# Kernel optimization log

Hardware: AMD Instinct MI355X
Metric: run time of the kernel (lower is better)

Reference implementation:

```python
import jax, jax.numpy as jnp
import numpy as np

LEAK = 0.01  # PyTorch LeakyReLU default negative_slope


def _leaky(x):
    return jnp.where(x >= 0, x, LEAK * x)


def _sim1(x, ws):
    # 7-layer 1x1-conv MLP applied per pixel; x: (..., Cin, H, W)
    n = len(ws)
    for i, w in enumerate(ws):
        x = jnp.einsum('oc,...chw->...ohw', w, x)
        if i < n - 1:
            x = _leaky(x)
    return x


def setup_inputs() -> dict:
    key = jax.random.key(0)
    ks = jax.random.split(key, 9)
    B, C, S, K = 8, 256, 15, 17
    d = {
        'template_feature': jax.random.normal(ks[0], (B, C, S, S), jnp.float32),
        'candidate_feature': jax.random.normal(ks[1], (B, C, S + K - 1, S + K - 1), jnp.float32),
    }
    chans = [(C, 2 * C), (C // 2, C), (C // 4, C // 2), (C // 8, C // 4),
             (C // 16, C // 8), (C // 32, C // 16), (1, C // 32)]
    for i, (o, c) in enumerate(chans):
        # kaiming_normal_ fan_out for a 1x1 conv: std = sqrt(2/out_channels)
        d[f'w{i}'] = jax.random.normal(ks[2 + i], (o, c), jnp.float32) * np.sqrt(2.0 / o).astype(np.float32)
    return d


def reference(template_feature, candidate_feature, w0, w1, w2, w3, w4, w5, w6):
    ws = (w0, w1, w2, w3, w4, w5, w6)
    B, C, S, _ = template_feature.shape
    K = 17  # sliding-window grid (31-15+1)

    # ---- template branch ----
    t_mean = jnp.mean(template_feature, axis=(-2, -1), keepdims=True)
    rep = jnp.concatenate([jnp.broadcast_to(t_mean, template_feature.shape),
                           template_feature], axis=1)  # (B, 2C, S, S)
    w = _sim1(rep, ws)  # (B, 1, S, S)
    wn = jax.nn.softmax(w.reshape(B, 1, -1), axis=2).reshape(B, 1, S, S)
    common_template = jnp.sum(template_feature * wn, axis=(-2, -1)).reshape(B, C, 1, 1)

    # ---- candidate branch: im2col of 15x15 windows over 31x31 -> 17x17 grid ----
    ii = jnp.arange(S)[:, None] + jnp.arange(K)[None, :]  # (S, K): in-window + window-offset
    # cand_all[b,c,i,j,p,q] = candidate[b,c, i+p, j+q]  -> (B, C, S, S, K, K)
    cand_all = candidate_feature[:, :, ii[:, None, :, None], ii[None, :, None, :]]
    c_mean = jnp.mean(cand_all, axis=(2, 3), keepdims=True)  # divide by S*S as in original
    rep_c = jnp.concatenate([jnp.broadcast_to(c_mean, cand_all.shape), cand_all], axis=1)  # (B, 2C, S, S, K, K)
    rep_c = jnp.transpose(rep_c, (0, 4, 5, 1, 2, 3))  # (B, K, K, 2C, S, S)
    w_c = _sim1(rep_c, ws)  # (B, K, K, 1, S, S)
    wcn = jax.nn.softmax(w_c.reshape(B, K, K, 1, -1), axis=-1).reshape(B, K, K, 1, S, S)
    wcn = jnp.transpose(wcn, (0, 3, 4, 5, 1, 2))  # (B, 1, S, S, K, K)
    common_candidate = jnp.sum(cand_all * wcn, axis=(2, 3))  # (B, C, K, K)

    return common_template, common_candidate
```

## Files before the change

kernel.cpp:

```cpp
#include <hip/hip_runtime.h>

typedef _Float16 half_t;
typedef half_t h2    __attribute__((ext_vector_type(2)));
typedef half_t half4 __attribute__((ext_vector_type(4)));
typedef half_t half8 __attribute__((ext_vector_type(8)));
typedef __fp16 pk16x2 __attribute__((ext_vector_type(2)));
typedef float  f32x4 __attribute__((ext_vector_type(4)));
typedef float  f32x2 __attribute__((ext_vector_type(2)));

static __device__ __forceinline__ half4 pack4(f32x4 a) {
  pk16x2 lo = __builtin_amdgcn_cvt_pkrtz(a[0], a[1]);
  pk16x2 hi = __builtin_amdgcn_cvt_pkrtz(a[2], a[3]);
  half4 h;
  h[0] = lo[0]; h[1] = lo[1]; h[2] = hi[0]; h[3] = hi[1];
  return h;
}

constexpr int B_  = 8;
constexpr int S_  = 15;
constexpr int K_  = 17;
constexpr int P_  = 31;
constexpr int SS_ = 225;
constexpr int PP_ = 961;
constexpr int KK_ = 289;

constexpr int NROW_C = B_ * PP_;
constexpr int NROW_T = B_ * SS_;
constexpr int NROW   = NROW_C + NROW_T;

constexpr int NW0H = 512 * 256;
constexpr int NF16 = 128*256 + 64*128 + 32*64;

constexpr size_t OFF_GOUT = 0;
constexpr size_t OFF_ROWS = OFF_GOUT + (size_t)NROW * 256;
constexpr size_t OFF_M0   = OFF_ROWS + (size_t)B_ * 31 * 17 * 256;
constexpr size_t OFF_TM0  = OFF_M0   + (size_t)B_ * KK_ * 256;
constexpr size_t OFF_F16  = OFF_TM0  + (size_t)B_ * 256;

constexpr int X0B  = 0;
constexpr int X1B  = 32768;
constexpr int X3TB = 32768;
constexpr int Y4B  = 41984;
constexpr int SMB  = 49152;
constexpr int REDB = 50112;
constexpr int W4B  = 50176;
constexpr int W5B  = 52480;
constexpr int W6B  = 53120;
constexpr int ROWB = 53152;
constexpr int LDSB = 53632;

__global__ __launch_bounds__(256) void featT_kernel(
    const float* __restrict__ templ, const float* __restrict__ cand,
    half_t* __restrict__ inarrh)
{
  __shared__ float tile[32 * 257];
  const int bid = blockIdx.x;
  const float* src;
  int base, npos, rowbase;
  if (bid < B_ * 31) {
    int b = bid / 31, ch = bid % 31;
    src = cand + (size_t)b * 256 * PP_;
    base = ch * 32; npos = min(32, PP_ - base);
    rowbase = b * PP_ + base;
  } else {
    int t = bid - B_ * 31;
    int b = t / 8, ch = t % 8;
    src = templ + (size_t)b * 256 * SS_;
    base = ch * 32; npos = min(32, SS_ - base);
    rowbase = NROW_C + b * SS_ + base;
  }
  const int tid = threadIdx.x;
  const int p  = tid & 31;
  const int c8 = tid >> 5;
  const int stride = (bid < B_ * 31) ? PP_ : SS_;
  if (p < npos) {
    for (int it = 0; it < 32; ++it) {
      int c = c8 * 32 + it;
      tile[p * 257 + c] = src[(size_t)c * stride + base + p];
    }
  }
  __syncthreads();
  for (int pp = 0; pp < npos; ++pp)
    inarrh[(size_t)(rowbase + pp) * 256 + tid] = (half_t)tile[pp * 257 + tid];
}

__global__ __launch_bounds__(256) void wcvt_kernel(
    const float* __restrict__ w0, const float* __restrict__ w1,
    const float* __restrict__ w2, const float* __restrict__ w3,
    half_t* __restrict__ w0h, half_t* __restrict__ w1h,
    half_t* __restrict__ w2h, half_t* __restrict__ w3h)
{
  const int total = NW0H + NF16;
  for (int idx = blockIdx.x * blockDim.x + threadIdx.x; idx < total;
       idx += gridDim.x * blockDim.x) {
    if (idx < NW0H) {
      int m = idx >> 8; int c = idx & 255;
      w0h[idx] = (half_t)(m < 256 ? w0[m * 512 + 256 + c] : w0[(m - 256) * 512 + c]);
    } else {
      int t = idx - NW0H;
      if (t < 32768)      w1h[t] = (half_t)w1[t];
      else if (t < 40960) w2h[t - 32768] = (half_t)w2[t - 32768];
      else                w3h[t - 40960] = (half_t)w3[t - 40960];
    }
  }
}

__global__ __launch_bounds__(512) void l0gemm_kernel(
    const half_t* __restrict__ inh, const half_t* __restrict__ w0h,
    half_t* __restrict__ conv1h, float* __restrict__ gout)
{
  __shared__ __align__(16) char xls[16 * 512];
  const int tid  = threadIdx.x;
  const int lane = tid & 63;
  const int wvs  = tid >> 6;
  const int row0 = blockIdx.x * 16;

  {
    const int row = tid >> 5;
    const int c8  = (tid & 31) * 8;
    half8 h = *(const half8*)(inh + (size_t)(row0 + row) * 256 + c8);
    const int off = (row * 512 + c8 * 2) ^ ((row & 7) << 4);
    *(half8*)(xls + off) = h;
  }
  __syncthreads();

  const int l15 = lane & 15, g = lane >> 4;
  f32x4 acc[4];
#pragma unroll
  for (int mt = 0; mt < 4; ++mt) acc[mt] = (f32x4){0.f, 0.f, 0.f, 0.f};
#pragma unroll 2
  for (int kb = 0; kb < 8; ++kb) {
    const int off = (l15 * 512 + kb * 64 + g * 16) ^ ((l15 & 7) << 4);
    half8 bfr = *(const half8*)(xls + off);
#pragma unroll
    for (int mt = 0; mt < 4; ++mt) {
      const half_t* ap = w0h + (size_t)((wvs * 4 + mt) * 16 + l15) * 256 + kb * 32 + g * 8;
      half8 a = *(const half8*)ap;
      acc[mt] = __builtin_amdgcn_mfma_f32_16x16x32_f16(a, bfr, acc[mt], 0, 0, 0);
    }
  }
#pragma unroll
  for (int mt = 0; mt < 4; ++mt) {
    const int m0c = (wvs * 4 + mt) * 16 + g * 4;
    if (wvs < 4)
      *(half4*)(conv1h + (size_t)(row0 + l15) * 256 + m0c) = pack4(acc[mt]);
    else
      *(f32x4*)(gout + (size_t)(row0 + l15) * 256 + (m0c - 256)) = acc[mt];
  }
}

__global__ __launch_bounds__(256) void rowsum_kernel(
    const float* __restrict__ gout, float* __restrict__ rows)
{
  const int bid = blockIdx.x;
  const int o = threadIdx.x;
  const int v = bid % 17; const int p = (bid / 17) % 31; const int b = bid / (17 * 31);
  float s = 0.f;
  for (int j = 0; j < 15; ++j)
    s += gout[(size_t)(b * PP_ + p * P_ + v + j) * 256 + o];
  rows[(size_t)bid * 256 + o] = s;
}

__global__ __launch_bounds__(256) void colsum_kernel(
    const float* __restrict__ rows, float* __restrict__ m0v)
{
  const int bid = blockIdx.x;
  const int o = threadIdx.x;
  const int v = bid % 17; const int u = (bid / 17) % 17; const int b = bid / KK_;
  float s = 0.f;
  for (int i = 0; i < 15; ++i)
    s += rows[(size_t)((b * 31 + u + i) * 17 + v) * 256 + o];
  m0v[(size_t)bid * 256 + o] = s * (1.0f / 225.0f);
}

__global__ __launch_bounds__(256) void tmean0_kernel(
    const float* __restrict__ gout, float* __restrict__ tm0v)
{
  const int b = blockIdx.x;
  const int o = threadIdx.x;
  float s = 0.f;
  for (int t = 0; t < SS_; ++t)
    s += gout[(size_t)(NROW_C + b * SS_ + t) * 256 + o];
  tm0v[b * 256 + o] = s * (1.0f / 225.0f);
}

__global__ __launch_bounds__(512, 4) void chain_kernel(
    const half_t* __restrict__ conv1h, const float* __restrict__ m0v,
    const float* __restrict__ tm0v,
    const half_t* __restrict__ w1h, const half_t* __restrict__ w2h,
    const half_t* __restrict__ w3h,
    const float* __restrict__ w4, const float* __restrict__ w5,
    const float* __restrict__ w6,
    const half_t* __restrict__ inarrh, float* __restrict__ out)
{
  __shared__ __align__(16) char lds[LDSB];
  float*    ldsf   = (float*)lds;
  float*    sm     = (float*)(lds + SMB);
  float*    red    = (float*)(lds + REDB);
  uint16_t* rowoff = (uint16_t*)(lds + ROWB);

  const int tid  = threadIdx.x;
  const int lane = tid & 63;
  const int wvs  = __builtin_amdgcn_readfirstlane(tid >> 6);
  const int bid  = (blockIdx.x & 7) * 290 + (blockIdx.x >> 3);
  const bool is_t = (bid >= B_ * KK_);
  int b, u = 0, v = 0;
  const float* mean_vec;
  if (!is_t) {
    b = bid / KK_;
    int r = bid % KK_;
    u = r / K_; v = r % K_;
    mean_vec = m0v + (size_t)bid * 256;
  } else {
    b = bid - B_ * KK_;
    mean_vec = tm0v + (size_t)b * 256;
  }

  if (tid < SS_) {
    int i = tid / 15, j = tid - i * 15;
    rowoff[tid] = is_t ? (uint16_t)(NROW_C + b * SS_ + tid)
                       : (uint16_t)(b * PP_ + (u + i) * P_ + (v + j));
  }
  ((float*)(lds + W4B))[(tid >> 5) * 36 + (tid & 31)] = w4[tid];
  if (tid < 128) ((float*)(lds + W5B))[(tid >> 4) * 20 + (tid & 15)] = w5[tid];
  if (tid < 8)   ((float*)(lds + W6B))[tid] = w6[tid];

  const half_t* w1base = w1h + (size_t)(16 * wvs + (lane & 15)) * 256 + ((lane >> 4) << 3);
  const int g2 = wvs & 3, h2w = wvs >> 2;
  half8 af2[4];
  {
    const half_t* base = w2h + (size_t)(16 * g2 + (lane & 15)) * 128 + ((lane >> 4) << 3);
#pragma unroll
    for (int kb = 0; kb < 4; ++kb) af2[kb] = *(const half8*)(base + kb * 32);
  }
  const int rt3 = wvs & 1, ct3 = wvs >> 1;
  const half_t* b3ptr = w3h + (size_t)(16 * rt3 + (lane & 15)) * 64 + ((lane >> 4) << 3);
  const int c8  = (lane & 31) * 8;
  const int lhi = lane >> 5;
  half8 mvh;
  {
    f32x4 ma = *(const f32x4*)(mean_vec + c8);
    f32x4 mb = *(const f32x4*)(mean_vec + c8 + 4);
    half4 h0 = pack4(ma), h1 = pack4(mb);
#pragma unroll
    for (int r = 0; r < 4; ++r) { mvh[r] = h0[r]; mvh[4 + r] = h1[r]; }
  }
  __syncthreads();

  for (int ti = 0; ti < 4; ++ti) {
    const int s0 = ti * 64;
    const int cnt = min(64, SS_ - s0);

    for (int it = 0; it < 4; ++it) {
      const int pos = 8 * wvs + it * 2 + lhi;
      const int srow = rowoff[min(s0 + pos, SS_ - 1)];
      half8 cv = *(const half8*)(conv1h + ((size_t)srow << 8) + c8);
      half8 t = cv + mvh;
      half8 s2 = t * (half_t)0.01f;
      half8 r8 = __builtin_elementwise_max(t, s2);
      const int off = (pos * 512 + c8 * 2) ^ ((pos & 7) << 4);
      *(half8*)(lds + X0B + off) = r8;
    }
    __syncthreads();

    f32x4 acc[4];
#pragma unroll
    for (int nt = 0; nt < 4; ++nt) acc[nt] = (f32x4){0.f, 0.f, 0.f, 0.f};
    {
      const half_t* w1p = w1base;
      asm volatile("" : "+v"(w1p));
#pragma unroll 2
      for (int kb = 0; kb < 8; ++kb) {
        half8 a1 = *(const half8*)(w1p + kb * 32);
        const int kbyte = kb * 64 + ((lane >> 4) << 4);
#pragma unroll
        for (int nt = 0; nt < 4; ++nt) {
          const int pos = nt * 16 + (lane & 15);
          const int off = (pos * 512 + kbyte) ^ ((pos & 7) << 4);
          half8 bfr = *(const half8*)(lds + X0B + off);
          acc[nt] = __builtin_amdgcn_mfma_f32_16x16x32_f16(a1, bfr, acc[nt], 0, 0, 0);
        }
      }
#pragma unroll
      for (int nt = 0; nt < 4; ++nt) {
        const int pos = nt * 16 + (lane & 15);
        f32x4 a;
#pragma unroll
        for (int r = 0; r < 4; ++r) a[r] = fmaxf(acc[nt][r], 0.01f * acc[nt][r]);
        const int ch0 = 16 * wvs + ((lane >> 4) << 2);
        const int off = (pos * 256 + ch0 * 2) ^ ((pos & 7) << 4);
        *(half4*)(lds + X1B + off) = pack4(a);
      }
    }
    __syncthreads();

    f32x4 acc2[2];
#pragma unroll
    for (int nt = 0; nt < 2; ++nt) acc2[nt] = (f32x4){0.f, 0.f, 0.f, 0.f};
#pragma unroll
    for (int kb = 0; kb < 4; ++kb) {
      const int kbyte = kb * 64 + ((lane >> 4) << 4);
#pragma unroll
      for (int nt = 0; nt < 2; ++nt) {
        const int pos = h2w * 32 + nt * 16 + (lane & 15);
        const int off = (pos * 256 + kbyte) ^ ((pos & 7) << 4);
        half8 bfr = *(const half8*)(lds + X1B + off);
        acc2[nt] = __builtin_amdgcn_mfma_f32_16x16x32_f16(af2[kb], bfr, acc2[nt], 0, 0, 0);
      }
    }
#pragma unroll
    for (int nt = 0; nt < 2; ++nt) {
      const int pos = h2w * 32 + nt * 16 + (lane & 15);
      const int ch0 = 16 * g2 + ((lane >> 4) << 2);
      f32x4 a;
#pragma unroll
      for (int r = 0; r < 4; ++r) a[r] = fmaxf(acc2[nt][r], 0.01f * acc2[nt][r]);
      const int off = (pos * 128 + ch0 * 2) ^ ((pos & 7) << 4);
      *(half4*)(lds + X0B + off) = pack4(a);
    }
    __syncthreads();

    {
      f32x4 acc3 = (f32x4){0.f, 0.f, 0.f, 0.f};
      const int pos = ct3 * 16 + (lane & 15);
#pragma unroll
      for (int kb = 0; kb < 2; ++kb) {
        half8 a3 = *(const half8*)(b3ptr + kb * 32);
        const int kbyte = kb * 64 + ((lane >> 4) << 4);
        const int off = (pos * 128 + kbyte) ^ ((pos & 7) << 4);
        half8 bfr = *(const half8*)(lds + X0B + off);
        acc3 = __builtin_amdgcn_mfma_f32_16x16x32_f16(a3, bfr, acc3, 0, 0, 0);
      }
      const int ch0 = 16 * rt3 + ((lane >> 4) << 2);
      f32x4 o4;
#pragma unroll
      for (int r = 0; r < 4; ++r) o4[r] = fmaxf(acc3[r], 0.01f * acc3[r]);
      *(f32x4*)(lds + X3TB + pos * 144 + ch0 * 4) = o4;
    }
    __syncthreads();

    {
      const int p = lane >> 3, g = lane & 7;
      const int pos = 8 * wvs + p;
      float a4_0 = 0.f, a4_1 = 0.f;
#pragma unroll
      for (int c0 = 0; c0 < 32; c0 += 4) {
        f32x4 x  = *(const f32x4*)(lds + X3TB + pos * 144 + c0 * 4);
        f32x4 wA = *(const f32x4*)(lds + W4B + (2 * g) * 144 + c0 * 4);
        f32x4 wB = *(const f32x4*)(lds + W4B + (2 * g + 1) * 144 + c0 * 4);
#pragma unroll
        for (int r = 0; r < 4; ++r) {
          a4_0 = fmaf(wA[r], x[r], a4_0);
          a4_1 = fmaf(wB[r], x[r], a4_1);
        }
      }
      f32x2 y4v;
      y4v[0] = fmaxf(a4_0, 0.01f * a4_0);
      y4v[1] = fmaxf(a4_1, 0.01f * a4_1);
      *(f32x2*)(lds + Y4B + pos * 80 + g * 8) = y4v;
      float a5 = 0.f;
#pragma unroll
      for (int c0 = 0; c0 < 16; c0 += 4) {
        f32x4 x = *(const f32x4*)(lds + Y4B + pos * 80 + c0 * 4);
        f32x4 w = *(const f32x4*)(lds + W5B + g * 80 + c0 * 4);
#pragma unroll
        for (int r = 0; r < 4; ++r) a5 = fmaf(w[r], x[r], a5);
      }
      a5 = fmaxf(a5, 0.01f * a5);
      float t6 = ((float*)(lds + W6B))[g] * a5;
      t6 += __shfl_xor(t6, 1);
      t6 += __shfl_xor(t6, 2);
      t6 += __shfl_xor(t6, 4);
      if (g == 0 && (8 * wvs + p) < cnt) sm[s0 + pos] = t6;
    }
    __syncthreads();
  }

  float vv = (tid < SS_) ? sm[tid] : -1e30f;
  float m = vv;
#pragma unroll
  for (int off = 32; off >= 1; off >>= 1) m = fmaxf(m, __shfl_xor(m, off));
  if (lane == 0) red[wvs] = m;
  __syncthreads();
  m = red[0];
#pragma unroll
  for (int w = 1; w < 8; ++w) m = fmaxf(m, red[w]);
  float e = (tid < SS_) ? __expf(vv - m) : 0.f;
  float ss = e;
#pragma unroll
  for (int off = 32; off >= 1; off >>= 1) ss += __shfl_xor(ss, off);
  __syncthreads();
  if (lane == 0) red[wvs] = ss;
  __syncthreads();
  float Stot = red[0];
#pragma unroll
  for (int w = 1; w < 8; ++w) Stot += red[w];
  if (tid < SS_) sm[tid] = e / Stot;
  __syncthreads();

  {
    const int c2 = (tid & 127) * 2;
    const int q  = tid >> 7;
    float accx = 0.f, accy = 0.f;
    for (int s = q; s < SS_; s += 4) {
      h2 ft = *(const h2*)(inarrh + ((size_t)rowoff[s] << 8) + c2);
      float w = sm[s];
      accx = fmaf(w, (float)ft[0], accx);
      accy = fmaf(w, (float)ft[1], accy);
    }
    __syncthreads();
    ldsf[q * 256 + c2]     = accx;
    ldsf[q * 256 + c2 + 1] = accy;
    __syncthreads();
    if (tid < 256) {
      float tot = ldsf[tid] + ldsf[256 + tid] + ldsf[512 + tid] + ldsf[768 + tid];
      if (!is_t) out[2048 + ((size_t)(b * 256 + tid) * 17 + u) * 17 + v] = tot;
      else       out[b * 256 + tid] = tot;
    }
  }
}

extern "C" void kernel_launch(void* const* d_in, const int* in_sizes, int n_in,
                              void* d_out, int out_size, void* d_ws, size_t ws_size,
                              hipStream_t stream)
{
  const float* templ = (const float*)d_in[0];
  const float* cand  = (const float*)d_in[1];
  const float* w0 = (const float*)d_in[2];
  const float* w1 = (const float*)d_in[3];
  const float* w2 = (const float*)d_in[4];
  const float* w3 = (const float*)d_in[5];
  const float* w4 = (const float*)d_in[6];
  const float* w5 = (const float*)d_in[7];
  const float* w6 = (const float*)d_in[8];

  float* ws    = (float*)d_ws;
  float* gout  = ws + OFF_GOUT;
  float* rows  = ws + OFF_ROWS;
  float* m0v   = ws + OFF_M0;
  float* tm0v  = ws + OFF_TM0;
  half_t* inarrh = (half_t*)(ws + OFF_F16);
  half_t* conv1h = inarrh + (size_t)NROW * 256;
  half_t* w0h  = conv1h + (size_t)NROW * 256;
  half_t* w1h  = w0h + NW0H;
  half_t* w2h  = w1h + 128 * 256;
  half_t* w3h  = w2h + 64 * 128;
  float* outf  = (float*)d_out;

  featT_kernel<<<B_ * 31 + B_ * 8, 256, 0, stream>>>(templ, cand, inarrh);
  wcvt_kernel<<<256, 256, 0, stream>>>(w0, w1, w2, w3, w0h, w1h, w2h, w3h);
  l0gemm_kernel<<<NROW / 16, 512, 0, stream>>>(inarrh, w0h, conv1h, gout);
  rowsum_kernel<<<B_ * 31 * 17, 256, 0, stream>>>(gout, rows);
  colsum_kernel<<<B_ * KK_, 256, 0, stream>>>(rows, m0v);
  tmean0_kernel<<<B_, 256, 0, stream>>>(gout, tm0v);
  chain_kernel<<<B_ * KK_ + B_, 512, 0, stream>>>(conv1h, m0v, tm0v,
                                                  w1h, w2h, w3h, w4, w5, w6,
                                                  inarrh, outf);
}
```

Before: 269.0 us.

## Merge prep and reduction kernels, prefetch next conv1 tile in chain kernel

Merges the feature-transpose and weight-conversion kernels into one launch, and the column-sum and template-mean kernels into another, cutting two kernel launches and their gaps. Inside the chain kernel, the global loads for the next 64-position tile are issued before the layer-4/5/6 epilogue and written to LDS after it, so the load latency overlaps compute and one barrier per tile goes away. This raises register pressure in a kernel bounded to 4 blocks per CU, and the weight-conversion work now runs on fewer blocks (88 instead of 256).

```diff
diff --git a/kernel.cpp b/kernel.cpp
--- a/kernel.cpp
+++ b/kernel.cpp
@@ -30,6 +30,7 @@
 
 constexpr int NW0H = 512 * 256;
 constexpr int NF16 = 128*256 + 64*128 + 32*64;
+constexpr int NFEATB = B_ * 31 + B_ * 8;
 
 constexpr size_t OFF_GOUT = 0;
 constexpr size_t OFF_ROWS = OFF_GOUT + (size_t)NROW * 256;
@@ -49,58 +50,57 @@
 constexpr int ROWB = 53152;
 constexpr int LDSB = 53632;
 
-__global__ __launch_bounds__(256) void featT_kernel(
+__global__ __launch_bounds__(256) void prep_kernel(
     const float* __restrict__ templ, const float* __restrict__ cand,
-    half_t* __restrict__ inarrh)
+    const float* __restrict__ w0, const float* __restrict__ w1,
+    const float* __restrict__ w2, const float* __restrict__ w3,
+    half_t* __restrict__ inarrh, half_t* __restrict__ w0h,
+    half_t* __restrict__ w1h, half_t* __restrict__ w2h,
+    half_t* __restrict__ w3h)
 {
   __shared__ float tile[32 * 257];
   const int bid = blockIdx.x;
-  const float* src;
-  int base, npos, rowbase;
-  if (bid < B_ * 31) {
-    int b = bid / 31, ch = bid % 31;
-    src = cand + (size_t)b * 256 * PP_;
-    base = ch * 32; npos = min(32, PP_ - base);
-    rowbase = b * PP_ + base;
+  const int tid = threadIdx.x;
+  if (bid < NFEATB) {
+    const float* src;
+    int base, npos, rowbase, stride;
+    if (bid < B_ * 31) {
+      int b = bid / 31, ch = bid % 31;
+      src = cand + (size_t)b * 256 * PP_;
+      base = ch * 32; npos = min(32, PP_ - base);
+      rowbase = b * PP_ + base; stride = PP_;
+    } else {
+      int t = bid - B_ * 31;
+      int b = t / 8, ch = t % 8;
+      src = templ + (size_t)b * 256 * SS_;
+      base = ch * 32; npos = min(32, SS_ - base);
+      rowbase = NROW_C + b * SS_ + base; stride = SS_;
+    }
+    const int p  = tid & 31;
+    const int c8 = tid >> 5;
+    if (p < npos) {
+      for (int it = 0; it < 32; ++it) {
+        int c = c8 * 32 + it;
+        tile[p * 257 + c] = src[(size_t)c * stride + base + p];
+      }
+    }
+    __syncthreads();
+    for (int pp = 0; pp < npos; ++pp)
+      inarrh[(size_t)(rowbase + pp) * 256 + tid] = (half_t)tile[pp * 257 + tid];
   } else {
-    int t = bid - B_ * 31;
-    int b = t / 8, ch = t % 8;
-    src = templ + (size_t)b * 256 * SS_;
-    base = ch * 32; npos = min(32, SS_ - base);
-    rowbase = NROW_C + b * SS_ + base;
-  }
-  const int tid = threadIdx.x;
-  const int p  = tid & 31;
-  const int c8 = tid >> 5;
-  const int stride = (bid < B_ * 31) ? PP_ : SS_;
-  if (p < npos) {
-    for (int it = 0; it < 32; ++it) {
-      int c = c8 * 32 + it;
-      tile[p * 257 + c] = src[(size_t)c * stride + base + p];
-    }
-  }
-  __syncthreads();
-  for (int pp = 0; pp < npos; ++pp)
-    inarrh[(size_t)(rowbase + pp) * 256 + tid] = (half_t)tile[pp * 257 + tid];
-}
-
-__global__ __launch_bounds__(256) void wcvt_kernel(
-    const float* __restrict__ w0, const float* __restrict__ w1,
-    const float* __restrict__ w2, const float* __restrict__ w3,
-    half_t* __restrict__ w0h, half_t* __restrict__ w1h,
-    half_t* __restrict__ w2h, half_t* __restrict__ w3h)
-{
-  const int total = NW0H + NF16;
-  for (int idx = blockIdx.x * blockDim.x + threadIdx.x; idx < total;
-       idx += gridDim.x * blockDim.x) {
-    if (idx < NW0H) {
-      int m = idx >> 8; int c = idx & 255;
-      w0h[idx] = (half_t)(m < 256 ? w0[m * 512 + 256 + c] : w0[(m - 256) * 512 + c]);
-    } else {
-      int t = idx - NW0H;
-      if (t < 32768)      w1h[t] = (half_t)w1[t];
-      else if (t < 40960) w2h[t - 32768] = (half_t)w2[t - 32768];
-      else                w3h[t - 40960] = (half_t)w3[t - 40960];
+    const int nb = gridDim.x - NFEATB;
+    const int wb = bid - NFEATB;
+    const int total = NW0H + NF16;
+    for (int idx = wb * 256 + tid; idx < total; idx += nb * 256) {
+      if (idx < NW0H) {
+        int m = idx >> 8; int c = idx & 255;
+        w0h[idx] = (half_t)(m < 256 ? w0[m * 512 + 256 + c] : w0[(m - 256) * 512 + c]);
+      } else {
+        int t = idx - NW0H;
+        if (t < 32768)      w1h[t] = (half_t)w1[t];
+        else if (t < 40960) w2h[t - 32768] = (half_t)w2[t - 32768];
+        else                w3h[t - 40960] = (half_t)w3[t - 40960];
+      }
     }
   }
 }
@@ -161,27 +161,25 @@
   rows[(size_t)bid * 256 + o] = s;
 }
 
-__global__ __launch_bounds__(256) void colsum_kernel(
-    const float* __restrict__ rows, float* __restrict__ m0v)
+__global__ __launch_bounds__(256) void colsum_tmean_kernel(
+    const float* __restrict__ rows, const float* __restrict__ gout,
+    float* __restrict__ m0v, float* __restrict__ tm0v)
 {
   const int bid = blockIdx.x;
   const int o = threadIdx.x;
-  const int v = bid % 17; const int u = (bid / 17) % 17; const int b = bid / KK_;
-  float s = 0.f;
-  for (int i = 0; i < 15; ++i)
-    s += rows[(size_t)((b * 31 + u + i) * 17 + v) * 256 + o];
-  m0v[(size_t)bid * 256 + o] = s * (1.0f / 225.0f);
-}
-
-__global__ __launch_bounds__(256) void tmean0_kernel(
-    const float* __restrict__ gout, float* __restrict__ tm0v)
-{
-  const int b = blockIdx.x;
-  const int o = threadIdx.x;
-  float s = 0.f;
-  for (int t = 0; t < SS_; ++t)
-    s += gout[(size_t)(NROW_C + b * SS_ + t) * 256 + o];
-  tm0v[b * 256 + o] = s * (1.0f / 225.0f);
+  if (bid < B_ * KK_) {
+    const int v = bid % 17; const int u = (bid / 17) % 17; const int b = bid / KK_;
+    float s = 0.f;
+    for (int i = 0; i < 15; ++i)
+      s += rows[(size_t)((b * 31 + u + i) * 17 + v) * 256 + o];
+    m0v[(size_t)bid * 256 + o] = s * (1.0f / 225.0f);
+  } else {
+    const int b = bid - B_ * KK_;
+    float s = 0.f;
+    for (int t = 0; t < SS_; ++t)
+      s += gout[(size_t)(NROW_C + b * SS_ + t) * 256 + o];
+    tm0v[b * 256 + o] = s * (1.0f / 225.0f);
+  }
 }
 
 __global__ __launch_bounds__(512, 4) void chain_kernel(
@@ -247,21 +245,29 @@
   }
   __syncthreads();
 
+  auto stage_write = [&](int pos, half8 cv) {
+    half8 t = cv + mvh;
+    half8 s2 = t * (half_t)0.01f;
+    half8 r8 = __builtin_elementwise_max(t, s2);
+    const int off = (pos * 512 + c8 * 2) ^ ((pos & 7) << 4);
+    *(half8*)(lds + X0B + off) = r8;
+  };
+
+  {
+    const int pbase = 8 * wvs + lhi;
+#pragma unroll
+    for (int it = 0; it < 4; ++it) {
+      const int pos = pbase + it * 2;
+      const int srow = rowoff[min(pos, SS_ - 1)];
+      half8 cv = *(const half8*)(conv1h + ((size_t)srow << 8) + c8);
+      stage_write(pos, cv);
+    }
+  }
+  __syncthreads();
+
   for (int ti = 0; ti < 4; ++ti) {
     const int s0 = ti * 64;
     const int cnt = min(64, SS_ - s0);
-
-    for (int it = 0; it < 4; ++it) {
-      const int pos = 8 * wvs + it * 2 + lhi;
-      const int srow = rowoff[min(s0 + pos, SS_ - 1)];
-      half8 cv = *(const half8*)(conv1h + ((size_t)srow << 8) + c8);
-      half8 t = cv + mvh;
-      half8 s2 = t * (half_t)0.01f;
-      half8 r8 = __builtin_elementwise_max(t, s2);
-      const int off = (pos * 512 + c8 * 2) ^ ((pos & 7) << 4);
-      *(half8*)(lds + X0B + off) = r8;
-    }
-    __syncthreads();
 
     f32x4 acc[4];
 #pragma unroll
@@ -340,6 +346,16 @@
     __syncthreads();
 
     {
+      half8 cv0, cv1, cv2, cv3;
+      const int pbase = 8 * wvs + lhi;
+      if (ti < 3) {
+        const int s1 = s0 + 64;
+        cv0 = *(const half8*)(conv1h + ((size_t)rowoff[min(s1 + pbase,     SS_ - 1)] << 8) + c8);
+        cv1 = *(const half8*)(conv1h + ((size_t)rowoff[min(s1 + pbase + 2, SS_ - 1)] << 8) + c8);
+        cv2 = *(const half8*)(conv1h + ((size_t)rowoff[min(s1 + pbase + 4, SS_ - 1)] << 8) + c8);
+        cv3 = *(const half8*)(conv1h + ((size_t)rowoff[min(s1 + pbase + 6, SS_ - 1)] << 8) + c8);
+      }
+
       const int p = lane >> 3, g = lane & 7;
       const int pos = 8 * wvs + p;
       float a4_0 = 0.f, a4_1 = 0.f;
@@ -371,7 +387,14 @@
       t6 += __shfl_xor(t6, 1);
       t6 += __shfl_xor(t6, 2);
       t6 += __shfl_xor(t6, 4);
-      if (g == 0 && (8 * wvs + p) < cnt) sm[s0 + pos] = t6;
+      if (g == 0 && pos < cnt) sm[s0 + pos] = t6;
+
+      if (ti < 3) {
+        stage_write(pbase,     cv0);
+        stage_write(pbase + 2, cv1);
+        stage_write(pbase + 4, cv2);
+        stage_write(pbase + 6, cv3);
+      }
     }
     __syncthreads();
   }
@@ -447,12 +470,11 @@
   half_t* w3h  = w2h + 64 * 128;
   float* outf  = (float*)d_out;
 
-  featT_kernel<<<B_ * 31 + B_ * 8, 256, 0, stream>>>(templ, cand, inarrh);
-  wcvt_kernel<<<256, 256, 0, stream>>>(w0, w1, w2, w3, w0h, w1h, w2h, w3h);
+  prep_kernel<<<NFEATB + 88, 256, 0, stream>>>(templ, cand, w0, w1, w2, w3,
+                                               inarrh, w0h, w1h, w2h, w3h);
   l0gemm_kernel<<<NROW / 16, 512, 0, stream>>>(inarrh, w0h, conv1h, gout);
   rowsum_kernel<<<B_ * 31 * 17, 256, 0, stream>>>(gout, rows);
-  colsum_kernel<<<B_ * KK_, 256, 0, stream>>>(rows, m0v);
-  tmean0_kernel<<<B_, 256, 0, stream>>>(gout, tm0v);
+  colsum_tmean_kernel<<<B_ * KK_ + B_, 256, 0, stream>>>(rows, gout, m0v, tm0v);
   chain_kernel<<<B_ * KK_ + B_, 512, 0, stream>>>(conv1h, m0v, tm0v,
                                                   w1h, w2h, w3h, w4, w5, w6,
                                                   inarrh, outf);
```

Measured after the change: 256.6 us. 4.6% less time.
